# Kernel optimization log

Measured on AMD Instinct MI355X. Metric: run time of the kernel, lower is better.

Reference implementation:

```python
import jax, jax.numpy as jnp
import numpy as np

EPS = 1e-08


def setup_inputs() -> dict:
    key = jax.random.key(0)
    k1, k2 = jax.random.split(key)
    B, K, H = 8, 8000, 512
    inputs = jax.random.normal(k1, (B, K, H), dtype=jnp.float32)
    gamma = jax.random.normal(k2, (1, H), dtype=jnp.float32) * 0.05  # 'random_normal' init
    beta = jnp.zeros((1, H), dtype=jnp.float32)
    return {"inputs": inputs, "gamma": gamma, "beta": beta}


def reference(inputs, gamma, beta):
    # Cumulative (causal) layer norm: at step k, normalize frame k using
    # mean/var computed over the prefix inputs[:, :k+1, :] (time and feature dims).
    B, K, H = inputs.shape
    # Running sums over time of per-frame sums across features -> O(K) scan.
    step_sum = jnp.sum(inputs, axis=-1)          # [B, K]
    step_sumsq = jnp.sum(inputs * inputs, axis=-1)  # [B, K]
    cum_sum = jnp.cumsum(step_sum, axis=1)       # [B, K]
    cum_sumsq = jnp.cumsum(step_sumsq, axis=1)   # [B, K]
    count = (jnp.arange(1, K + 1, dtype=inputs.dtype) * H)  # [K] elements in each prefix
    mean = cum_sum / count                        # [B, K]
    var = cum_sumsq / count - mean * mean         # [B, K]
    inv_std = 1.0 / jnp.sqrt(var + EPS)           # matches (var + eps) ** 0.5
    # gamma/beta: (1, H) broadcast over [B, K, H]
    out = gamma * ((inputs - mean[..., None]) * inv_std[..., None]) + beta
    return out
```

## Files before the change

kernel.cpp:

```cpp
#include <hip/hip_runtime.h>
#include <math.h>


#define HDIM 512
#define F4H (HDIM / 4)
#define SEG 64
#define BATCHES 8
#define KLEN 8000
#define SEGS (KLEN / SEG)
#define NBLK (BATCHES * SEGS)

typedef float f32x4 __attribute__((ext_vector_type(4)));
typedef unsigned long long u64;

__global__ __launch_bounds__(256, 4) void cln_fused1(
    const float* __restrict__ in, const float* __restrict__ gamma,
    const float* __restrict__ beta, float* __restrict__ out,
    double* __restrict__ segS, double* __restrict__ segQ,
    unsigned int* __restrict__ done)
{
    __shared__ f32x4 stage[16][F4H];
    __shared__ float fsum[SEG], fsq[SEG], meanS[SEG], istdS[SEG];
    __shared__ double wS[4], wQ[4];

    const int tid  = threadIdx.x;
    const int lane = tid & 63;
    const int wid  = tid >> 6;
    const int bx   = blockIdx.x;
    const int b    = bx / SEGS;
    const int s    = bx % SEGS;
    const int k0   = s * SEG;

    const f32x4 g0  = ((const f32x4*)gamma)[lane];
    const f32x4 g1  = ((const f32x4*)gamma)[lane + 64];
    const f32x4 be0 = ((const f32x4*)beta)[lane];
    const f32x4 be1 = ((const f32x4*)beta)[lane + 64];

    const f32x4* p = (const f32x4*)in + ((size_t)b * KLEN + k0 + wid * 16) * F4H;

    f32x4 xa[4], xc[4];
    double accS = 0.0, accQ = 0.0;
    #pragma unroll
    for (int fi = 0; fi < 16; ++fi) {
        const f32x4 a = p[(size_t)fi * F4H + lane];
        const f32x4 c = p[(size_t)fi * F4H + 64 + lane];
        float sv = (a.x + a.y) + (a.z + a.w) + (c.x + c.y) + (c.z + c.w);
        float qv = (a.x * a.x + a.y * a.y) + (a.z * a.z + a.w * a.w)
                 + (c.x * c.x + c.y * c.y) + (c.z * c.z + c.w * c.w);
        #pragma unroll
        for (int off = 32; off >= 1; off >>= 1) {
            sv += __shfl_xor(sv, off);
            qv += __shfl_xor(qv, off);
        }
        if (lane == 0) { fsum[wid * 16 + fi] = sv; fsq[wid * 16 + fi] = qv; }
        accS += (double)sv;
        accQ += (double)qv;
        if (fi < 4) {
            stage[wid * 4 + fi][lane]      = a;
            stage[wid * 4 + fi][64 + lane] = c;
        } else if (fi < 8) {
            xa[fi - 4] = a; xc[fi - 4] = c;
        }
    }
    if (lane == 0) { wS[wid] = accS; wQ[wid] = accQ; }
    __syncthreads();
    if (tid == 0) {
        const double S = wS[0] + wS[1] + wS[2] + wS[3];
        const double Q = wQ[0] + wQ[1] + wQ[2] + wQ[3];
        __hip_atomic_store((u64*)&segS[bx], __double_as_longlong(S),
                           __ATOMIC_RELAXED, __HIP_MEMORY_SCOPE_AGENT);
        __hip_atomic_store((u64*)&segQ[bx], __double_as_longlong(Q),
                           __ATOMIC_RELAXED, __HIP_MEMORY_SCOPE_AGENT);
        __hip_atomic_fetch_add(&done[b], 1u,
                               __ATOMIC_RELEASE, __HIP_MEMORY_SCOPE_AGENT);
        while (__hip_atomic_load(&done[b], __ATOMIC_ACQUIRE,
                                 __HIP_MEMORY_SCOPE_AGENT) < (unsigned)SEGS)
            __builtin_amdgcn_s_sleep(32);
    }
    __syncthreads();

    if (wid == 0) {
        double es = 0.0, eq = 0.0;
        for (int base = 0; base < s; base += 64) {
            const int j = base + lane;
            if (j < s) {
                es += __longlong_as_double(__hip_atomic_load(
                        (u64*)&segS[b * SEGS + j],
                        __ATOMIC_RELAXED, __HIP_MEMORY_SCOPE_AGENT));
                eq += __longlong_as_double(__hip_atomic_load(
                        (u64*)&segQ[b * SEGS + j],
                        __ATOMIC_RELAXED, __HIP_MEMORY_SCOPE_AGENT));
            }
        }
        #pragma unroll
        for (int off = 32; off >= 1; off >>= 1) {
            es += __shfl_xor(es, off);
            eq += __shfl_xor(eq, off);
        }
        double sc = (double)fsum[lane], qc = (double)fsq[lane];
        #pragma unroll
        for (int off = 1; off < 64; off <<= 1) {
            double s2 = __shfl_up(sc, off);
            double q2 = __shfl_up(qc, off);
            if (lane >= off) { sc += s2; qc += q2; }
        }
        sc += es; qc += eq;
        const double cnt = (double)(k0 + lane + 1) * (double)HDIM;
        const double m   = sc / cnt;
        const double var = qc / cnt - m * m;
        meanS[lane] = (float)m;
        istdS[lane] = (float)(1.0 / sqrt(var + 1e-8));
    }
    __syncthreads();

    f32x4* o4 = (f32x4*)out + ((size_t)b * KLEN + k0 + wid * 16) * F4H;

#define APPLY(fi, a, c) {                                                   \
        const float m = meanS[wid * 16 + (fi)];                             \
        const float r = istdS[wid * 16 + (fi)];                             \
        f32x4 o0, o1;                                                       \
        o0.x = g0.x * ((a.x - m) * r) + be0.x;                              \
        o0.y = g0.y * ((a.y - m) * r) + be0.y;                              \
        o0.z = g0.z * ((a.z - m) * r) + be0.z;                              \
        o0.w = g0.w * ((a.w - m) * r) + be0.w;                              \
        o1.x = g1.x * ((c.x - m) * r) + be1.x;                              \
        o1.y = g1.y * ((c.y - m) * r) + be1.y;                              \
        o1.z = g1.z * ((c.z - m) * r) + be1.z;                              \
        o1.w = g1.w * ((c.w - m) * r) + be1.w;                              \
        __builtin_nontemporal_store(o0, o4 + (size_t)(fi) * F4H + lane);    \
        __builtin_nontemporal_store(o1, o4 + (size_t)(fi) * F4H + 64 + lane); }

    #pragma unroll
    for (int fi = 8; fi < 16; ++fi) {
        const f32x4 a = p[(size_t)fi * F4H + lane];
        const f32x4 c = p[(size_t)fi * F4H + 64 + lane];
        APPLY(fi, a, c);
    }
    #pragma unroll
    for (int fi = 4; fi < 8; ++fi) {
        APPLY(fi, xa[fi - 4], xc[fi - 4]);
    }
    #pragma unroll
    for (int fi = 0; fi < 4; ++fi) {
        const f32x4 a = stage[wid * 4 + fi][lane];
        const f32x4 c = stage[wid * 4 + fi][64 + lane];
        APPLY(fi, a, c);
    }
#undef APPLY
}

__global__ __launch_bounds__(256) void k_seg_sums(
    const float* __restrict__ in, float* __restrict__ ssum,
    float* __restrict__ ssq, double* __restrict__ segS,
    double* __restrict__ segQ, int K, int segsPerBatch)
{
    const int lane = threadIdx.x & 63;
    const int wid  = threadIdx.x >> 6;
    const int segGlobal = blockIdx.x;
    const int b   = segGlobal / segsPerBatch;
    const int seg = segGlobal % segsPerBatch;
    const int k0  = seg * SEG;

    double accS = 0.0, accQ = 0.0;
    #pragma unroll 4
    for (int i = 0; i < SEG / 4; ++i) {
        const int fk = k0 + wid * (SEG / 4) + i;
        if (fk < K) {
            const float4* p = (const float4*)in + ((size_t)b * K + fk) * F4H;
            float4 a = p[lane];
            float4 c = p[lane + 64];
            float s = (a.x + a.y) + (a.z + a.w) + (c.x + c.y) + (c.z + c.w);
            float q = (a.x * a.x + a.y * a.y) + (a.z * a.z + a.w * a.w)
                    + (c.x * c.x + c.y * c.y) + (c.z * c.z + c.w * c.w);
            #pragma unroll
            for (int off = 32; off >= 1; off >>= 1) {
                s += __shfl_xor(s, off);
                q += __shfl_xor(q, off);
            }
            if (lane == 0) {
                ssum[(size_t)b * K + fk] = s;
                ssq[(size_t)b * K + fk]  = q;
            }
            accS += (double)s;
            accQ += (double)q;
        }
    }
    __shared__ double wS[4], wQ[4];
    if (lane == 0) { wS[wid] = accS; wQ[wid] = accQ; }
    __syncthreads();
    if (threadIdx.x == 0) {
        segS[segGlobal] = wS[0] + wS[1] + wS[2] + wS[3];
        segQ[segGlobal] = wQ[0] + wQ[1] + wQ[2] + wQ[3];
    }
}

__global__ __launch_bounds__(256) void k_norm_fused(
    const float* __restrict__ in, const float* __restrict__ gamma,
    const float* __restrict__ beta, const float* __restrict__ ssum,
    const float* __restrict__ ssq, const double* __restrict__ segS,
    const double* __restrict__ segQ, float* __restrict__ out,
    int K, int segsPerBatch)
{
    __shared__ float meanS[SEG], istdS[SEG];

    const int tid  = threadIdx.x;
    const int lane = tid & 63;
    const int wid  = tid >> 6;
    const int b = blockIdx.x / segsPerBatch;
    const int s = blockIdx.x % segsPerBatch;
    const int k0 = s * SEG;

    const f32x4 g0  = ((const f32x4*)gamma)[lane];
    const f32x4 g1  = ((const f32x4*)gamma)[lane + 64];
    const f32x4 be0 = ((const f32x4*)beta)[lane];
    const f32x4 be1 = ((const f32x4*)beta)[lane + 64];

    if (wid == 0) {
        double es = 0.0, eq = 0.0;
        for (int base = 0; base < s; base += 64) {
            const int j = base + lane;
            if (j < s) {
                es += segS[(size_t)b * segsPerBatch + j];
                eq += segQ[(size_t)b * segsPerBatch + j];
            }
        }
        #pragma unroll
        for (int off = 32; off >= 1; off >>= 1) {
            es += __shfl_xor(es, off);
            eq += __shfl_xor(eq, off);
        }
        const int k = k0 + lane;
        double sc = 0.0, qc = 0.0;
        if (k < K) {
            sc = (double)ssum[(size_t)b * K + k];
            qc = (double)ssq[(size_t)b * K + k];
        }
        #pragma unroll
        for (int off = 1; off < 64; off <<= 1) {
            double s2 = __shfl_up(sc, off);
            double q2 = __shfl_up(qc, off);
            if (lane >= off) { sc += s2; qc += q2; }
        }
        sc += es; qc += eq;
        if (k < K) {
            const double cnt = (double)(k + 1) * (double)HDIM;
            const double m   = sc / cnt;
            const double var = qc / cnt - m * m;
            meanS[lane] = (float)m;
            istdS[lane] = (float)(1.0 / sqrt(var + 1e-8));
        }
    }
    __syncthreads();

    #pragma unroll 4
    for (int i = 0; i < SEG / 4; ++i) {
        const int fi = wid * (SEG / 4) + i;
        const int k = k0 + fi;
        if (k < K) {
            const f32x4* p = (const f32x4*)in + ((size_t)b * K + k) * F4H;
            const f32x4 a = p[lane];
            const f32x4 c = p[lane + 64];
            const float m = meanS[fi];
            const float r = istdS[fi];
            f32x4 o0, o1;
            o0.x = g0.x * ((a.x - m) * r) + be0.x;
            o0.y = g0.y * ((a.y - m) * r) + be0.y;
            o0.z = g0.z * ((a.z - m) * r) + be0.z;
            o0.w = g0.w * ((a.w - m) * r) + be0.w;
            o1.x = g1.x * ((c.x - m) * r) + be1.x;
            o1.y = g1.y * ((c.y - m) * r) + be1.y;
            o1.z = g1.z * ((c.z - m) * r) + be1.z;
            o1.w = g1.w * ((c.w - m) * r) + be1.w;
            f32x4* q = (f32x4*)out + ((size_t)b * K + k) * F4H;
            __builtin_nontemporal_store(o0, q + lane);
            __builtin_nontemporal_store(o1, q + lane + 64);
        }
    }
}

extern "C" void kernel_launch(void* const* d_in, const int* in_sizes, int n_in,
                              void* d_out, int out_size, void* d_ws, size_t ws_size,
                              hipStream_t stream)
{
    const float* in    = (const float*)d_in[0];
    const float* gamma = (const float*)d_in[1];
    const float* beta  = (const float*)d_in[2];
    float* out = (float*)d_out;

    const int H = in_sizes[1];
    const int BK = in_sizes[0] / H;
    const int K = BK / BATCHES;
    const int segsPerBatch = (K + SEG - 1) / SEG;
    const int NSEG = BATCHES * segsPerBatch;
    (void)n_in; (void)out_size; (void)ws_size;

    double* segS = (double*)d_ws;
    double* segQ = segS + NSEG;
    unsigned int* done = (unsigned int*)(segQ + NSEG);
    float* ssum = (float*)(done + 16);
    float* ssq  = ssum + BK;

    bool fused = (H == HDIM) && (K == KLEN) && (BK == BATCHES * KLEN);
    if (fused) {
        int dev = 0, nb = 0, cus = 0;
        if (hipGetDevice(&dev) != hipSuccess) fused = false;
        if (fused && hipOccupancyMaxActiveBlocksPerMultiprocessor(
                        &nb, (const void*)cln_fused1, 256, 0) != hipSuccess)
            fused = false;
        if (fused && hipDeviceGetAttribute(&cus, hipDeviceAttributeMultiprocessorCount,
                                           dev) != hipSuccess) fused = false;
        if (fused && (long)nb * cus < NBLK) fused = false;
    }

    if (fused) {
        hipMemsetAsync(done, 0, 16 * sizeof(unsigned int), stream);
        cln_fused1<<<dim3(NBLK), dim3(256), 0, stream>>>(
            in, gamma, beta, out, segS, segQ, done);
    } else {
        k_seg_sums<<<dim3(NSEG), dim3(256), 0, stream>>>(
            in, ssum, ssq, segS, segQ, K, segsPerBatch);
        k_norm_fused<<<dim3(NSEG), dim3(256), 0, stream>>>(
            in, gamma, beta, ssum, ssq, segS, segQ, out, K, segsPerBatch);
    }
}
```

Measured before the change: 66.95 us.

## Replace grid-wide barrier with decoupled lookback using per-segment flags and virtual block IDs

```diff
diff --git a/kernel.cpp b/kernel.cpp
--- a/kernel.cpp
+++ b/kernel.cpp
@@ -13,37 +13,44 @@
 typedef float f32x4 __attribute__((ext_vector_type(4)));
 typedef unsigned long long u64;
 
-__global__ __launch_bounds__(256, 4) void cln_fused1(
+__global__ __launch_bounds__(1024) void cln_pipe(
     const float* __restrict__ in, const float* __restrict__ gamma,
     const float* __restrict__ beta, float* __restrict__ out,
     double* __restrict__ segS, double* __restrict__ segQ,
-    unsigned int* __restrict__ done)
+    unsigned int* __restrict__ flags, unsigned int* __restrict__ vidctr)
 {
-    __shared__ f32x4 stage[16][F4H];
+    extern __shared__ f32x4 xs[];
     __shared__ float fsum[SEG], fsq[SEG], meanS[SEG], istdS[SEG];
-    __shared__ double wS[4], wQ[4];
+    __shared__ double wS[16], wQ[16];
+    __shared__ unsigned int vid_s;
 
     const int tid  = threadIdx.x;
     const int lane = tid & 63;
     const int wid  = tid >> 6;
-    const int bx   = blockIdx.x;
-    const int b    = bx / SEGS;
-    const int s    = bx % SEGS;
-    const int k0   = s * SEG;
+
+    if (tid == 0) vid_s = atomicAdd(vidctr, 1u);
+    __syncthreads();
+    const unsigned int vid = vid_s;
+    const int b = vid & (BATCHES - 1);
+    const int s = vid >> 3;
+    const int k0 = s * SEG;
+    const int me = b * SEGS + s;
 
     const f32x4 g0  = ((const f32x4*)gamma)[lane];
     const f32x4 g1  = ((const f32x4*)gamma)[lane + 64];
     const f32x4 be0 = ((const f32x4*)beta)[lane];
     const f32x4 be1 = ((const f32x4*)beta)[lane + 64];
 
-    const f32x4* p = (const f32x4*)in + ((size_t)b * KLEN + k0 + wid * 16) * F4H;
-
-    f32x4 xa[4], xc[4];
+    const f32x4* p = (const f32x4*)in + ((size_t)b * KLEN + k0) * F4H;
+
     double accS = 0.0, accQ = 0.0;
     #pragma unroll
-    for (int fi = 0; fi < 16; ++fi) {
-        const f32x4 a = p[(size_t)fi * F4H + lane];
-        const f32x4 c = p[(size_t)fi * F4H + 64 + lane];
+    for (int i = 0; i < 4; ++i) {
+        const int f = wid * 4 + i;
+        const f32x4 a = p[(size_t)f * F4H + lane];
+        const f32x4 c = p[(size_t)f * F4H + 64 + lane];
+        xs[f * F4H + lane]      = a;
+        xs[f * F4H + 64 + lane] = c;
         float sv = (a.x + a.y) + (a.z + a.w) + (c.x + c.y) + (c.z + c.w);
         float qv = (a.x * a.x + a.y * a.y) + (a.z * a.z + a.w * a.w)
                  + (c.x * c.x + c.y * c.y) + (c.z * c.z + c.w * c.w);
@@ -52,43 +59,44 @@
             sv += __shfl_xor(sv, off);
             qv += __shfl_xor(qv, off);
         }
-        if (lane == 0) { fsum[wid * 16 + fi] = sv; fsq[wid * 16 + fi] = qv; }
+        if (lane == 0) { fsum[f] = sv; fsq[f] = qv; }
         accS += (double)sv;
         accQ += (double)qv;
-        if (fi < 4) {
-            stage[wid * 4 + fi][lane]      = a;
-            stage[wid * 4 + fi][64 + lane] = c;
-        } else if (fi < 8) {
-            xa[fi - 4] = a; xc[fi - 4] = c;
-        }
     }
     if (lane == 0) { wS[wid] = accS; wQ[wid] = accQ; }
     __syncthreads();
+
     if (tid == 0) {
-        const double S = wS[0] + wS[1] + wS[2] + wS[3];
-        const double Q = wQ[0] + wQ[1] + wQ[2] + wQ[3];
-        __hip_atomic_store((u64*)&segS[bx], __double_as_longlong(S),
+        double S = 0.0, Q = 0.0;
+        #pragma unroll
+        for (int w = 0; w < 16; ++w) { S += wS[w]; Q += wQ[w]; }
+        __hip_atomic_store((u64*)&segS[me], __double_as_longlong(S),
                            __ATOMIC_RELAXED, __HIP_MEMORY_SCOPE_AGENT);
-        __hip_atomic_store((u64*)&segQ[bx], __double_as_longlong(Q),
+        __hip_atomic_store((u64*)&segQ[me], __double_as_longlong(Q),
                            __ATOMIC_RELAXED, __HIP_MEMORY_SCOPE_AGENT);
-        __hip_atomic_fetch_add(&done[b], 1u,
-                               __ATOMIC_RELEASE, __HIP_MEMORY_SCOPE_AGENT);
-        while (__hip_atomic_load(&done[b], __ATOMIC_ACQUIRE,
-                                 __HIP_MEMORY_SCOPE_AGENT) < (unsigned)SEGS)
-            __builtin_amdgcn_s_sleep(32);
-    }
-    __syncthreads();
+        __hip_atomic_store(&flags[me], 1u,
+                           __ATOMIC_RELEASE, __HIP_MEMORY_SCOPE_AGENT);
+    }
 
     if (wid == 0) {
         double es = 0.0, eq = 0.0;
-        for (int base = 0; base < s; base += 64) {
+        #pragma unroll
+        for (int base = 0; base < SEGS; base += 64) {
             const int j = base + lane;
-            if (j < s) {
-                es += __longlong_as_double(__hip_atomic_load(
-                        (u64*)&segS[b * SEGS + j],
+            const bool need = (j < s);
+            const int idx = b * SEGS + (need ? j : 0);
+            unsigned int f;
+            do {
+                f = need ? __hip_atomic_load(&flags[idx], __ATOMIC_ACQUIRE,
+                                             __HIP_MEMORY_SCOPE_AGENT)
+                         : 1u;
+                if (__ballot(f == 0u) == 0ull) break;
+                __builtin_amdgcn_s_sleep(8);
+            } while (true);
+            if (need) {
+                es += __longlong_as_double(__hip_atomic_load((u64*)&segS[idx],
                         __ATOMIC_RELAXED, __HIP_MEMORY_SCOPE_AGENT));
-                eq += __longlong_as_double(__hip_atomic_load(
-                        (u64*)&segQ[b * SEGS + j],
+                eq += __longlong_as_double(__hip_atomic_load((u64*)&segQ[idx],
                         __ATOMIC_RELAXED, __HIP_MEMORY_SCOPE_AGENT));
             }
         }
@@ -113,40 +121,26 @@
     }
     __syncthreads();
 
-    f32x4* o4 = (f32x4*)out + ((size_t)b * KLEN + k0 + wid * 16) * F4H;
-
-#define APPLY(fi, a, c) {                                                   \
-        const float m = meanS[wid * 16 + (fi)];                             \
-        const float r = istdS[wid * 16 + (fi)];                             \
-        f32x4 o0, o1;                                                       \
-        o0.x = g0.x * ((a.x - m) * r) + be0.x;                              \
-        o0.y = g0.y * ((a.y - m) * r) + be0.y;                              \
-        o0.z = g0.z * ((a.z - m) * r) + be0.z;                              \
-        o0.w = g0.w * ((a.w - m) * r) + be0.w;                              \
-        o1.x = g1.x * ((c.x - m) * r) + be1.x;                              \
-        o1.y = g1.y * ((c.y - m) * r) + be1.y;                              \
-        o1.z = g1.z * ((c.z - m) * r) + be1.z;                              \
-        o1.w = g1.w * ((c.w - m) * r) + be1.w;                              \
-        __builtin_nontemporal_store(o0, o4 + (size_t)(fi) * F4H + lane);    \
-        __builtin_nontemporal_store(o1, o4 + (size_t)(fi) * F4H + 64 + lane); }
-
+    f32x4* o4 = (f32x4*)out + ((size_t)b * KLEN + k0) * F4H;
     #pragma unroll
-    for (int fi = 8; fi < 16; ++fi) {
-        const f32x4 a = p[(size_t)fi * F4H + lane];
-        const f32x4 c = p[(size_t)fi * F4H + 64 + lane];
-        APPLY(fi, a, c);
-    }
-    #pragma unroll
-    for (int fi = 4; fi < 8; ++fi) {
-        APPLY(fi, xa[fi - 4], xc[fi - 4]);
-    }
-    #pragma unroll
-    for (int fi = 0; fi < 4; ++fi) {
-        const f32x4 a = stage[wid * 4 + fi][lane];
-        const f32x4 c = stage[wid * 4 + fi][64 + lane];
-        APPLY(fi, a, c);
-    }
-#undef APPLY
+    for (int i = 0; i < 4; ++i) {
+        const int f = wid * 4 + i;
+        const float m = meanS[f];
+        const float r = istdS[f];
+        const f32x4 a = xs[f * F4H + lane];
+        const f32x4 c = xs[f * F4H + 64 + lane];
+        f32x4 o0, o1;
+        o0.x = g0.x * ((a.x - m) * r) + be0.x;
+        o0.y = g0.y * ((a.y - m) * r) + be0.y;
+        o0.z = g0.z * ((a.z - m) * r) + be0.z;
+        o0.w = g0.w * ((a.w - m) * r) + be0.w;
+        o1.x = g1.x * ((c.x - m) * r) + be1.x;
+        o1.y = g1.y * ((c.y - m) * r) + be1.y;
+        o1.z = g1.z * ((c.z - m) * r) + be1.z;
+        o1.w = g1.w * ((c.w - m) * r) + be1.w;
+        __builtin_nontemporal_store(o0, o4 + (size_t)f * F4H + lane);
+        __builtin_nontemporal_store(o1, o4 + (size_t)f * F4H + 64 + lane);
+    }
 }
 
 __global__ __launch_bounds__(256) void k_seg_sums(
@@ -296,26 +290,24 @@
 
     double* segS = (double*)d_ws;
     double* segQ = segS + NSEG;
-    unsigned int* done = (unsigned int*)(segQ + NSEG);
-    float* ssum = (float*)(done + 16);
+    unsigned int* flags  = (unsigned int*)(segQ + NSEG);
+    unsigned int* vidctr = flags + NSEG;
+    float* ssum = (float*)(vidctr + 16);
     float* ssq  = ssum + BK;
 
-    bool fused = (H == HDIM) && (K == KLEN) && (BK == BATCHES * KLEN);
-    if (fused) {
-        int dev = 0, nb = 0, cus = 0;
-        if (hipGetDevice(&dev) != hipSuccess) fused = false;
-        if (fused && hipOccupancyMaxActiveBlocksPerMultiprocessor(
-                        &nb, (const void*)cln_fused1, 256, 0) != hipSuccess)
-            fused = false;
-        if (fused && hipDeviceGetAttribute(&cus, hipDeviceAttributeMultiprocessorCount,
-                                           dev) != hipSuccess) fused = false;
-        if (fused && (long)nb * cus < NBLK) fused = false;
-    }
-
-    if (fused) {
-        hipMemsetAsync(done, 0, 16 * sizeof(unsigned int), stream);
-        cln_fused1<<<dim3(NBLK), dim3(256), 0, stream>>>(
-            in, gamma, beta, out, segS, segQ, done);
+    const size_t dynLds = (size_t)SEG * F4H * sizeof(f32x4);
+
+    bool pipe = (H == HDIM) && (K == KLEN) && (BK == BATCHES * KLEN);
+    if (pipe) {
+        if (hipFuncSetAttribute((const void*)cln_pipe,
+                hipFuncAttributeMaxDynamicSharedMemorySize,
+                (int)dynLds) != hipSuccess) pipe = false;
+    }
+
+    if (pipe) {
+        hipMemsetAsync(flags, 0, (NSEG + 16) * sizeof(unsigned int), stream);
+        cln_pipe<<<dim3(NBLK), dim3(1024), dynLds, stream>>>(
+            in, gamma, beta, out, segS, segQ, flags, vidctr);
     } else {
         k_seg_sums<<<dim3(NSEG), dim3(256), 0, stream>>>(
             in, ssum, ssq, segS, segQ, K, segsPerBatch);
```

New measurement: 86.15 us. +28.7%, slower.

## Replace per-batch barrier with per-segment flags for decoupled prefix waits

Applied to the files above, without the earlier changes.

```diff
diff --git a/kernel.cpp b/kernel.cpp
--- a/kernel.cpp
+++ b/kernel.cpp
@@ -13,11 +13,11 @@
 typedef float f32x4 __attribute__((ext_vector_type(4)));
 typedef unsigned long long u64;
 
-__global__ __launch_bounds__(256, 4) void cln_fused1(
+__global__ __launch_bounds__(256, 4) void cln_pipe2(
     const float* __restrict__ in, const float* __restrict__ gamma,
     const float* __restrict__ beta, float* __restrict__ out,
     double* __restrict__ segS, double* __restrict__ segQ,
-    unsigned int* __restrict__ done)
+    unsigned int* __restrict__ flags)
 {
     __shared__ f32x4 stage[16][F4H];
     __shared__ float fsum[SEG], fsq[SEG], meanS[SEG], istdS[SEG];
@@ -27,9 +27,10 @@
     const int lane = tid & 63;
     const int wid  = tid >> 6;
     const int bx   = blockIdx.x;
-    const int b    = bx / SEGS;
-    const int s    = bx % SEGS;
+    const int b    = bx & (BATCHES - 1);
+    const int s    = bx >> 3;
     const int k0   = s * SEG;
+    const int me   = b * SEGS + s;
 
     const f32x4 g0  = ((const f32x4*)gamma)[lane];
     const f32x4 g1  = ((const f32x4*)gamma)[lane + 64];
@@ -64,31 +65,37 @@
     }
     if (lane == 0) { wS[wid] = accS; wQ[wid] = accQ; }
     __syncthreads();
+
     if (tid == 0) {
         const double S = wS[0] + wS[1] + wS[2] + wS[3];
         const double Q = wQ[0] + wQ[1] + wQ[2] + wQ[3];
-        __hip_atomic_store((u64*)&segS[bx], __double_as_longlong(S),
+        __hip_atomic_store((u64*)&segS[me], __double_as_longlong(S),
                            __ATOMIC_RELAXED, __HIP_MEMORY_SCOPE_AGENT);
-        __hip_atomic_store((u64*)&segQ[bx], __double_as_longlong(Q),
+        __hip_atomic_store((u64*)&segQ[me], __double_as_longlong(Q),
                            __ATOMIC_RELAXED, __HIP_MEMORY_SCOPE_AGENT);
-        __hip_atomic_fetch_add(&done[b], 1u,
-                               __ATOMIC_RELEASE, __HIP_MEMORY_SCOPE_AGENT);
-        while (__hip_atomic_load(&done[b], __ATOMIC_ACQUIRE,
-                                 __HIP_MEMORY_SCOPE_AGENT) < (unsigned)SEGS)
-            __builtin_amdgcn_s_sleep(32);
-    }
-    __syncthreads();
+        __hip_atomic_store(&flags[me], 1u,
+                           __ATOMIC_RELEASE, __HIP_MEMORY_SCOPE_AGENT);
+    }
 
     if (wid == 0) {
         double es = 0.0, eq = 0.0;
-        for (int base = 0; base < s; base += 64) {
+        #pragma unroll
+        for (int base = 0; base < SEGS; base += 64) {
             const int j = base + lane;
-            if (j < s) {
-                es += __longlong_as_double(__hip_atomic_load(
-                        (u64*)&segS[b * SEGS + j],
+            const bool need = (j < s);
+            const int idx = b * SEGS + (need ? j : 0);
+            for (;;) {
+                const unsigned int f =
+                    need ? __hip_atomic_load(&flags[idx], __ATOMIC_ACQUIRE,
+                                             __HIP_MEMORY_SCOPE_AGENT)
+                         : 1u;
+                if (__ballot(f == 0u) == 0ull) break;
+                __builtin_amdgcn_s_sleep(8);
+            }
+            if (need) {
+                es += __longlong_as_double(__hip_atomic_load((u64*)&segS[idx],
                         __ATOMIC_RELAXED, __HIP_MEMORY_SCOPE_AGENT));
-                eq += __longlong_as_double(__hip_atomic_load(
-                        (u64*)&segQ[b * SEGS + j],
+                eq += __longlong_as_double(__hip_atomic_load((u64*)&segQ[idx],
                         __ATOMIC_RELAXED, __HIP_MEMORY_SCOPE_AGENT));
             }
         }
@@ -296,26 +303,26 @@
 
     double* segS = (double*)d_ws;
     double* segQ = segS + NSEG;
-    unsigned int* done = (unsigned int*)(segQ + NSEG);
-    float* ssum = (float*)(done + 16);
+    unsigned int* flags = (unsigned int*)(segQ + NSEG);
+    float* ssum = (float*)(flags + NSEG + 16);
     float* ssq  = ssum + BK;
 
-    bool fused = (H == HDIM) && (K == KLEN) && (BK == BATCHES * KLEN);
-    if (fused) {
+    bool pipe = (H == HDIM) && (K == KLEN) && (BK == BATCHES * KLEN);
+    if (pipe) {
         int dev = 0, nb = 0, cus = 0;
-        if (hipGetDevice(&dev) != hipSuccess) fused = false;
-        if (fused && hipOccupancyMaxActiveBlocksPerMultiprocessor(
-                        &nb, (const void*)cln_fused1, 256, 0) != hipSuccess)
-            fused = false;
-        if (fused && hipDeviceGetAttribute(&cus, hipDeviceAttributeMultiprocessorCount,
-                                           dev) != hipSuccess) fused = false;
-        if (fused && (long)nb * cus < NBLK) fused = false;
-    }
-
-    if (fused) {
-        hipMemsetAsync(done, 0, 16 * sizeof(unsigned int), stream);
-        cln_fused1<<<dim3(NBLK), dim3(256), 0, stream>>>(
-            in, gamma, beta, out, segS, segQ, done);
+        if (hipGetDevice(&dev) != hipSuccess) pipe = false;
+        if (pipe && hipOccupancyMaxActiveBlocksPerMultiprocessor(
+                        &nb, (const void*)cln_pipe2, 256, 0) != hipSuccess)
+            pipe = false;
+        if (pipe && hipDeviceGetAttribute(&cus, hipDeviceAttributeMultiprocessorCount,
+                                          dev) != hipSuccess) pipe = false;
+        if (pipe && (long)nb * cus < NBLK) pipe = false;
+    }
+
+    if (pipe) {
+        hipMemsetAsync(flags, 0, NSEG * sizeof(unsigned int), stream);
+        cln_pipe2<<<dim3(NBLK), dim3(256), 0, stream>>>(
+            in, gamma, beta, out, segS, segQ, flags);
     } else {
         k_seg_sums<<<dim3(NSEG), dim3(256), 0, stream>>>(
             in, ssum, ssq, segS, segQ, K, segsPerBatch);
```

New measurement: 66.94 us, median of 3. No clear change (-0.0%).
